# Kernel optimization log

Hardware: AMD Instinct MI355X
Metric: run time of the kernel (lower is better)

## Reference

```python
import jax, jax.numpy as jnp
import numpy as np

V, SMAX, D, L, H, F = 50257, 1024, 768, 12, 12, 3072
DH = D // H
SCALE = float(np.sqrt(DH))


def setup_inputs() -> dict:
    key = jax.random.key(0)
    ks = jax.random.split(key, 24)
    B, S = 2, 1024
    std = 0.02
    inp = {
        'input_ids': jax.random.randint(ks[0], (B, S), 0, V),
        'tok_emb': jax.random.normal(ks[1], (V, D), jnp.float32) * std,
        'pos_emb': jax.random.normal(ks[2], (SMAX, D), jnp.float32) * std,
        # stacked per-layer params (leading dim L)
        'Wq': jax.random.normal(ks[3], (L, D, D), jnp.float32) * std,
        'bq': jnp.zeros((L, D), jnp.float32),
        'Wk': jax.random.normal(ks[4], (L, D, D), jnp.float32) * std,
        'bk': jnp.zeros((L, D), jnp.float32),
        'Wv': jax.random.normal(ks[5], (L, D, D), jnp.float32) * std,
        'bv': jnp.zeros((L, D), jnp.float32),
        'Wo': jax.random.normal(ks[6], (L, D, D), jnp.float32) * std,
        'bo': jnp.zeros((L, D), jnp.float32),
        'ln1_g': jnp.ones((L, D), jnp.float32),
        'ln1_b': jnp.zeros((L, D), jnp.float32),
        'ln2_g': jnp.ones((L, D), jnp.float32),
        'ln2_b': jnp.zeros((L, D), jnp.float32),
        'W1': jax.random.normal(ks[7], (L, D, F), jnp.float32) * std,
        'b1': jnp.zeros((L, F), jnp.float32),
        'W2': jax.random.normal(ks[8], (L, F, D), jnp.float32) * std,
        'b2': jnp.zeros((L, D), jnp.float32),
        'lnf_g': jnp.ones((D,), jnp.float32),
        'lnf_b': jnp.zeros((D,), jnp.float32),
        'Whead': jax.random.normal(ks[9], (D, V), jnp.float32) * std,
    }
    return inp


def _layernorm(x, g, b, eps=1e-5):
    mu = jnp.mean(x, axis=-1, keepdims=True)
    var = jnp.var(x, axis=-1, keepdims=True)
    return (x - mu) * jax.lax.rsqrt(var + eps) * g + b


def _gpt_forward(input_ids, tok_emb, pos_emb, Wq, bq, Wk, bk, Wv, bv, Wo, bo,
                 ln1_g, ln1_b, ln2_g, ln2_b, W1, b1, W2, b2, lnf_g, lnf_b, Whead):
    B, S = input_ids.shape
    x = tok_emb[input_ids] + pos_emb[:S][None, :, :]  # (B,S,D)
    # additive causal mask: -inf above the diagonal
    idx = jnp.arange(S)
    neg_inf = jnp.finfo(x.dtype).min
    mask = jnp.where(idx[None, :] > idx[:, None], neg_inf, 0.0).astype(x.dtype)  # (S,S)

    def block(x, p):
        (wq, bq_, wk, bk_, wv, bv_, wo, bo_, g1, b1_, g2, b2_, w1, bb1, w2, bb2) = p
        h = _layernorm(x, g1, b1_)
        q = (h @ wq + bq_).reshape(B, S, H, DH)
        k = (h @ wk + bk_).reshape(B, S, H, DH)
        v = (h @ wv + bv_).reshape(B, S, H, DH)
        scores = jnp.einsum('bqhd,bkhd->bhqk', q, k) / SCALE + mask
        attn = jax.nn.softmax(scores, axis=-1)
        o = jnp.einsum('bhqk,bkhd->bqhd', attn, v).reshape(B, S, D)
        x = x + (o @ wo + bo_)
        h2 = _layernorm(x, g2, b2_)
        ffn = jax.nn.gelu(h2 @ w1 + bb1, approximate=False) @ w2 + bb2
        return x + ffn, None

    params = (Wq, bq, Wk, bk, Wv, bv, Wo, bo, ln1_g, ln1_b, ln2_g, ln2_b, W1, b1, W2, b2)
    x, _ = jax.lax.scan(block, x, params)
    x = _layernorm(x, lnf_g, lnf_b)
    return x @ Whead  # (B,S,V) logits


def reference(input_ids, tok_emb, pos_emb, Wq, bq, Wk, bk, Wv, bv, Wo, bo,
              ln1_g, ln1_b, ln2_g, ln2_b, W1, b1, W2, b2, lnf_g, lnf_b, Whead):
    return _gpt_forward(input_ids, tok_emb, pos_emb, Wq, bq, Wk, bk, Wv, bv, Wo, bo,
                        ln1_g, ln1_b, ln2_g, ln2_b, W1, b1, W2, b2, lnf_g, lnf_b, Whead)
```

## Files before the change

### kernel.cpp

```cpp
#include <hip/hip_runtime.h>
#include <hip/hip_bf16.h>
#include <cstdint>
#include <cstddef>

#define DEV __device__ __forceinline__

typedef __attribute__((ext_vector_type(8))) short short8;
typedef __attribute__((ext_vector_type(4))) short s16x4;
typedef __attribute__((ext_vector_type(4))) float f32x4;
typedef unsigned short u16;
typedef unsigned int u32;

static constexpr int Vv = 50257;
static constexpr int Dd = 768;
static constexpr int Ll = 12;
static constexpr int Hh = 12;
static constexpr int Ff = 3072;
static constexpr int Ss = 1024;
static constexpr int Bbatch = 2;
static constexpr int DHh = 64;
static constexpr int Mtok = Bbatch * Ss;
static constexpr int NQKV = 3 * Dd;
static constexpr int VPAD = 50304;

DEV u16 f2bf(float f){ u32 x; __builtin_memcpy(&x, &f, 4); x += 0x7fffu + ((x >> 16) & 1u); return (u16)(x >> 16); }

DEV void gld_lds16(const void* g, void* l){
  __builtin_amdgcn_global_load_lds((const __attribute__((address_space(1))) void*)g,
                                   (__attribute__((address_space(3))) void*)l, 16, 0, 0);
}

__global__ __launch_bounds__(256) void k_embed_ln(const int* __restrict__ ids, const float* __restrict__ tok,
                                                  const float* __restrict__ pos, const float* __restrict__ g,
                                                  const float* __restrict__ b, float* __restrict__ x,
                                                  u16* __restrict__ h){
  int t = blockIdx.x, tid = threadIdx.x;
  int id = ids[t];
  int s = t & (Ss - 1);
  const float* tr = tok + (size_t)id * Dd;
  const float* pr = pos + (size_t)s * Dd;
  float v0 = tr[tid] + pr[tid], v1 = tr[tid + 256] + pr[tid + 256], v2 = tr[tid + 512] + pr[tid + 512];
  float* xr = x + (size_t)t * Dd;
  xr[tid] = v0; xr[tid + 256] = v1; xr[tid + 512] = v2;
  float sm = v0 + v1 + v2, ss = v0 * v0 + v1 * v1 + v2 * v2;
  for (int o = 1; o < 64; o <<= 1){ sm += __shfl_xor(sm, o, 64); ss += __shfl_xor(ss, o, 64); }
  __shared__ float red[8];
  int w = tid >> 6, l = tid & 63;
  if (l == 0){ red[w] = sm; red[w + 4] = ss; }
  __syncthreads();
  sm = red[0] + red[1] + red[2] + red[3];
  ss = red[4] + red[5] + red[6] + red[7];
  float mu = sm * (1.0f / Dd);
  float var = ss * (1.0f / Dd) - mu * mu;
  float rs = rsqrtf(var + 1e-5f);
  u16* yr = h + (size_t)t * Dd;
  yr[tid]       = f2bf((v0 - mu) * rs * g[tid]       + b[tid]);
  yr[tid + 256] = f2bf((v1 - mu) * rs * g[tid + 256] + b[tid + 256]);
  yr[tid + 512] = f2bf((v2 - mu) * rs * g[tid + 512] + b[tid + 512]);
}

__global__ __launch_bounds__(256) void k_ln(const float* __restrict__ x, const float* __restrict__ g,
                                            const float* __restrict__ b, u16* __restrict__ y){
  int row = blockIdx.x, tid = threadIdx.x;
  const float* xr = x + (size_t)row * Dd;
  float v0 = xr[tid], v1 = xr[tid + 256], v2 = xr[tid + 512];
  float s = v0 + v1 + v2, ss = v0 * v0 + v1 * v1 + v2 * v2;
  for (int o = 1; o < 64; o <<= 1){ s += __shfl_xor(s, o, 64); ss += __shfl_xor(ss, o, 64); }
  __shared__ float red[8];
  int w = tid >> 6, l = tid & 63;
  if (l == 0){ red[w] = s; red[w + 4] = ss; }
  __syncthreads();
  s = red[0] + red[1] + red[2] + red[3];
  ss = red[4] + red[5] + red[6] + red[7];
  float mu = s * (1.0f / Dd);
  float var = ss * (1.0f / Dd) - mu * mu;
  float rs = rsqrtf(var + 1e-5f);
  u16* yr = y + (size_t)row * Dd;
  yr[tid]       = f2bf((v0 - mu) * rs * g[tid]       + b[tid]);
  yr[tid + 256] = f2bf((v1 - mu) * rs * g[tid + 256] + b[tid + 256]);
  yr[tid + 512] = f2bf((v2 - mu) * rs * g[tid + 512] + b[tid + 512]);
}

__global__ __launch_bounds__(256) void k_combineln(const float* __restrict__ p, const float* __restrict__ bias,
                                                   float* __restrict__ x, const float* __restrict__ g,
                                                   const float* __restrict__ b, u16* __restrict__ h){
  constexpr size_t SL = (size_t)Mtok * Dd;
  int row = blockIdx.x, tid = threadIdx.x;
  float* xr = x + (size_t)row * Dd;
  const float* p0 = p + (size_t)row * Dd;
  const float* p1 = p0 + SL;
  float v0 = xr[tid]       + p0[tid]       + p1[tid]       + bias[tid];
  float v1 = xr[tid + 256] + p0[tid + 256] + p1[tid + 256] + bias[tid + 256];
  float v2 = xr[tid + 512] + p0[tid + 512] + p1[tid + 512] + bias[tid + 512];
  xr[tid] = v0; xr[tid + 256] = v1; xr[tid + 512] = v2;
  float s = v0 + v1 + v2, ss = v0 * v0 + v1 * v1 + v2 * v2;
  for (int o = 1; o < 64; o <<= 1){ s += __shfl_xor(s, o, 64); ss += __shfl_xor(ss, o, 64); }
  __shared__ float red[8];
  int w = tid >> 6, l = tid & 63;
  if (l == 0){ red[w] = s; red[w + 4] = ss; }
  __syncthreads();
  s = red[0] + red[1] + red[2] + red[3];
  ss = red[4] + red[5] + red[6] + red[7];
  float mu = s * (1.0f / Dd);
  float var = ss * (1.0f / Dd) - mu * mu;
  float rs = rsqrtf(var + 1e-5f);
  u16* yr = h + (size_t)row * Dd;
  yr[tid]       = f2bf((v0 - mu) * rs * g[tid]       + b[tid]);
  yr[tid + 256] = f2bf((v1 - mu) * rs * g[tid + 256] + b[tid + 256]);
  yr[tid + 512] = f2bf((v2 - mu) * rs * g[tid + 512] + b[tid + 512]);
}

__global__ __launch_bounds__(256) void k_transpose(const float* __restrict__ src, u16* __restrict__ dst,
                                                   int R, int C, long smat, long dmat){
  __shared__ float tile[64][33];
  src += (size_t)blockIdx.z * smat;
  dst += (size_t)blockIdx.z * dmat;
  int c0 = blockIdx.x * 32, r0 = blockIdx.y * 64;
  int tid = threadIdx.x;
  int tc = tid & 31, tr = tid >> 5;
  #pragma unroll
  for (int i = 0; i < 8; i++){
    int r = tr + i * 8, c = c0 + tc;
    tile[r][tc] = (c < C) ? src[(size_t)(r0 + r) * C + c] : 0.0f;
  }
  __syncthreads();
  #pragma unroll
  for (int it = 0; it < 2; it++){
    int id = it * 256 + tid;
    int c = id & 31, rg = id >> 5, r = rg * 4;
    int cc = c0 + c;
    if (cc < C){
      s16x4 v = { (short)f2bf(tile[r][c]), (short)f2bf(tile[r + 1][c]),
                  (short)f2bf(tile[r + 2][c]), (short)f2bf(tile[r + 3][c]) };
      *(s16x4*)(dst + (size_t)cc * R + r0 + r) = v;
    }
  }
}

__global__ void k_biaspack(const float* __restrict__ bq, const float* __restrict__ bk,
                           const float* __restrict__ bv, float* __restrict__ o){
  int i = blockIdx.x * 256 + threadIdx.x;
  int col = i % NQKV, lay = i / NQKV;
  float v = (col < Dd) ? bq[lay * Dd + col]
          : (col < 2 * Dd) ? bk[lay * Dd + col - Dd]
          : bv[lay * Dd + col - 2 * Dd];
  o[i] = v;
}

template<int BM, int BN, int EPI>
__global__ __launch_bounds__(256) void k_gemmF(const u16* __restrict__ A, const u16* __restrict__ Bt,
    const float* __restrict__ bias, float* __restrict__ Cf, u16* __restrict__ Cb,
    u16* __restrict__ vt, int Nn, int MT, int NT){
  constexpr bool SPLIT = (EPI == 4);
  constexpr int KST  = SPLIT ? Ff : Dd;
  constexpr int KLEN = SPLIT ? (Ff / 2) : Dd;
  constexpr int nk = KLEN / 32;
  constexpr int HM = BM / 2, HN = BN / 2, FM = HM / 16, FN = HN / 16;
  constexpr int nA = (BM * 4) / 256, nB = (BN * 4) / 256;
  constexpr int ABYTE = BM * 64, BBYTE = BN * 64;
  __shared__ __align__(16) u16 ldsA[2 * BM * 32];
  __shared__ __align__(16) u16 ldsB[2 * BN * 32];
  int tid = threadIdx.x, wid = tid >> 6, l = tid & 63;
  int wm = wid >> 1, wn = wid & 1;
  int lr = l & 15, lc = l >> 4;
  int nwg = gridDim.x, dIdx = blockIdx.x;
  int L = (dIdx & 7) * (nwg >> 3) + (dIdx >> 3);
  int kidx = 0;
  if (SPLIT){ int per = MT * NT; kidx = L / per; L -= kidx * per; }
  int mtile = L % MT, ntile = L / MT;
  int m0 = mtile * BM, n0 = ntile * BN;
  int kbase = kidx * KLEN;

  const u16* gA[nA]; u16* dA[nA];
  const u16* gB[nB]; u16* dB[nB];
  #pragma unroll
  for (int i = 0; i < nA; i++){
    int id = i * 256 + tid, row = id >> 2, c = id & 3;
    int cs = c ^ ((row >> 1) & 3);
    gA[i] = A + (size_t)(m0 + row) * KST + kbase + cs * 8;
    dA[i] = ldsA + id * 8;
  }
  #pragma unroll
  for (int i = 0; i < nB; i++){
    int id = i * 256 + tid, row = id >> 2, c = id & 3;
    int cs = c ^ ((row >> 1) & 3);
    gB[i] = Bt + (size_t)(n0 + row) * KST + kbase + cs * 8;
    dB[i] = ldsB + id * 8;
  }
  int offA[FM], offB[FN];
  #pragma unroll
  for (int i = 0; i < FM; i++){
    int row = wm * HM + i * 16 + lr;
    offA[i] = row * 64 + ((lc ^ ((row >> 1) & 3)) << 4);
  }
  #pragma unroll
  for (int j = 0; j < FN; j++){
    int row = wn * HN + j * 16 + lr;
    offB[j] = row * 64 + ((lc ^ ((row >> 1) & 3)) << 4);
  }

  f32x4 acc[FM][FN];
  #pragma unroll
  for (int i = 0; i < FM; i++)
    #pragma unroll
    for (int j = 0; j < FN; j++) acc[i][j] = (f32x4)0.0f;

  auto stage = [&](int buf){
    #pragma unroll
    for (int i = 0; i < nA; i++){ gld_lds16(gA[i], (char*)dA[i] + buf * ABYTE); gA[i] += 32; }
    #pragma unroll
    for (int i = 0; i < nB; i++){ gld_lds16(gB[i], (char*)dB[i] + buf * BBYTE); gB[i] += 32; }
  };
  auto compute = [&](int buf){
    const char* bA = (const char*)ldsA + buf * ABYTE;
    const char* bB = (const char*)ldsB + buf * BBYTE;
    short8 af[FM], bfr[FN];
    #pragma unroll
    for (int i = 0; i < FM; i++) af[i] = *(const short8*)(bA + offA[i]);
    #pragma unroll
    for (int j = 0; j < FN; j++) bfr[j] = *(const short8*)(bB + offB[j]);
    #pragma unroll
    for (int i = 0; i < FM; i++)
      #pragma unroll
      for (int j = 0; j < FN; j++){
        if (EPI == 0)
          acc[i][j] = __builtin_amdgcn_mfma_f32_16x16x32_bf16(af[i], bfr[j], acc[i][j], 0, 0, 0);
        else
          acc[i][j] = __builtin_amdgcn_mfma_f32_16x16x32_bf16(bfr[j], af[i], acc[i][j], 0, 0, 0);
      }
  };

  stage(0);
  __syncthreads();
  #pragma unroll 1
  for (int t = 0; t < nk - 1; ++t){
    stage((t + 1) & 1);
    compute(t & 1);
    __syncthreads();
  }
  compute((nk - 1) & 1);

  if (EPI == 0){
    #pragma unroll
    for (int i = 0; i < FM; i++){
      #pragma unroll
      for (int j = 0; j < FN; j++){
        int col = n0 + wn * HN + j * 16 + lr;
        if (col >= Nn) continue;
        #pragma unroll
        for (int r = 0; r < 4; r++){
          int row = m0 + wm * HM + i * 16 + lc * 4 + r;
          Cf[(size_t)row * Nn + col] = acc[i][j][r];
        }
      }
    }
    return;
  }
  #pragma unroll
  for (int i = 0; i < FM; i++){
    int row = m0 + wm * HM + i * 16 + lr;
    #pragma unroll
    for (int j = 0; j < FN; j++){
      int c0 = n0 + wn * HN + j * 16 + lc * 4;
      f32x4 v = acc[i][j];
      if (EPI == 4){
        *(f32x4*)(Cf + (size_t)kidx * Mtok * Dd + (size_t)row * Dd + c0) = v;
        continue;
      }
      f32x4 bv = *(const f32x4*)(bias + c0);
      v = v + bv;
      if (EPI == 3){
        f32x4* p = (f32x4*)(Cf + (size_t)row * Nn + c0);
        *p = *p + v;
        continue;
      }
      if (EPI == 1 && c0 < Dd) v = v * 0.125f;
      if (EPI == 2){
        #pragma unroll
        for (int r = 0; r < 4; r++) v[r] = 0.5f * v[r] * (1.0f + erff(v[r] * 0.70710678118f));
      }
      u16 q0 = f2bf(v[0]), q1 = f2bf(v[1]), q2 = f2bf(v[2]), q3 = f2bf(v[3]);
      if (EPI == 1 && c0 >= 2 * Dd){
        int c2 = c0 - 2 * Dd, hh = c2 >> 6, dd2 = c2 & 63;
        int bb = row >> 10, ss2 = row & 1023;
        size_t base = ((size_t)((bb * Hh + hh) * DHh + dd2)) << 10;
        vt[base + ss2] = q0;
        vt[base + (1 << 10) + ss2] = q1;
        vt[base + (2 << 10) + ss2] = q2;
        vt[base + (3 << 10) + ss2] = q3;
      } else {
        s16x4 pv = { (short)q0, (short)q1, (short)q2, (short)q3 };
        *(s16x4*)(Cb + (size_t)row * Nn + c0) = pv;
      }
    }
  }
}

__global__ __launch_bounds__(256) void k_attn(const u16* __restrict__ qkv, const u16* __restrict__ vt,
                                              u16* __restrict__ o){
  __shared__ __align__(16) u16 ldsK[64 * 64];
  __shared__ __align__(16) u16 ldsV[64 * 64];
  __shared__ __align__(16) u16 ldsP[4][16 * 72];
  int bid = blockIdx.x;
  int iq = (Ss / 64) - 1 - (bid / (Bbatch * Hh));
  int bh = bid % (Bbatch * Hh);
  int b = bh / Hh, h = bh % Hh;
  int tid = threadIdx.x, wid = tid >> 6, l = tid & 63, lr = l & 15, lc = l >> 4;
  int nt = iq + 1;
  int qrow = b * Ss + iq * 64 + wid * 16 + lr;
  const u16* qp = qkv + (size_t)qrow * NQKV + h * DHh;
  short8 qf0 = *(const short8*)(qp + lc * 8);
  short8 qf1 = *(const short8*)(qp + 32 + lc * 8);

  const u16* gK[2]; const u16* gV[2]; u16* dK[2]; u16* dV[2];
  #pragma unroll
  for (int c = 0; c < 2; c++){
    int id = c * 256 + tid, row = id >> 3, ch = id & 7;
    int cs = ch ^ (row & 7);
    gK[c] = qkv + (size_t)(b * Ss + row) * NQKV + Dd + h * DHh + cs * 8;
    gV[c] = vt + ((size_t)(bh * DHh) + row) * Ss + cs * 8;
    dK[c] = ldsK + id * 8;
    dV[c] = ldsV + id * 8;
  }
  int koff[4][2];
  #pragma unroll
  for (int fn = 0; fn < 4; fn++){
    int kv = fn * 16 + lr;
    #pragma unroll
    for (int ks = 0; ks < 2; ks++){
      int ch = ks * 4 + lc;
      koff[fn][ks] = kv * 128 + ((ch ^ (kv & 7)) << 4);
    }
  }

  float mreg = -1e30f, lsum = 0.0f;
  f32x4 oacc[4];
  #pragma unroll
  for (int i = 0; i < 4; i++) oacc[i] = (f32x4)0.0f;
  u16* pbase = ldsP[wid];

  #pragma unroll 1
  for (int t = 0; t < nt; ++t){
    #pragma unroll
    for (int c = 0; c < 2; c++){ gld_lds16(gK[c], dK[c]); gK[c] += (size_t)64 * NQKV; }
    #pragma unroll
    for (int c = 0; c < 2; c++){ gld_lds16(gV[c], dV[c]); gV[c] += 64; }
    __syncthreads();
    f32x4 sc[4];
    __builtin_amdgcn_s_setprio(1);
    #pragma unroll
    for (int fn = 0; fn < 4; fn++){
      short8 kf0 = *(const short8*)((const char*)ldsK + koff[fn][0]);
      short8 kf1 = *(const short8*)((const char*)ldsK + koff[fn][1]);
      sc[fn] = __builtin_amdgcn_mfma_f32_16x16x32_bf16(kf0, qf0, (f32x4)0.0f, 0, 0, 0);
      sc[fn] = __builtin_amdgcn_mfma_f32_16x16x32_bf16(kf1, qf1, sc[fn], 0, 0, 0);
    }
    __builtin_amdgcn_s_setprio(0);
    if (t == iq){
      #pragma unroll
      for (int fn = 0; fn < 4; fn++)
        #pragma unroll
        for (int r = 0; r < 4; r++)
          if (fn * 16 + lc * 4 + r > wid * 16 + lr) sc[fn][r] = -1e30f;
    }
    float pm = sc[0][0];
    #pragma unroll
    for (int fn = 0; fn < 4; fn++)
      #pragma unroll
      for (int r = 0; r < 4; r++) pm = fmaxf(pm, sc[fn][r]);
    pm = fmaxf(pm, __shfl_xor(pm, 16, 64));
    pm = fmaxf(pm, __shfl_xor(pm, 32, 64));
    float mnew = fmaxf(mreg, pm);
    float alpha = __expf(mreg - mnew);
    mreg = mnew;
    float rs = 0.0f;
    #pragma unroll
    for (int fn = 0; fn < 4; fn++)
      #pragma unroll
      for (int r = 0; r < 4; r++){
        float p = __expf(sc[fn][r] - mnew);
        sc[fn][r] = p;
        rs += p;
      }
    rs += __shfl_xor(rs, 16, 64);
    rs += __shfl_xor(rs, 32, 64);
    lsum = lsum * alpha + rs;
    #pragma unroll
    for (int fn = 0; fn < 4; fn++){
      s16x4 pv = { (short)f2bf(sc[fn][0]), (short)f2bf(sc[fn][1]),
                   (short)f2bf(sc[fn][2]), (short)f2bf(sc[fn][3]) };
      *(s16x4*)((char*)pbase + lr * 144 + fn * 32 + lc * 8) = pv;
    }
    asm volatile("s_waitcnt lgkmcnt(0)" ::: "memory");
    __builtin_amdgcn_sched_barrier(0);
    #pragma unroll
    for (int fd = 0; fd < 4; fd++)
      #pragma unroll
      for (int r = 0; r < 4; r++) oacc[fd][r] *= alpha;
    short8 pa0 = *(const short8*)((const char*)pbase + lr * 144 + lc * 16);
    short8 pa1 = *(const short8*)((const char*)pbase + lr * 144 + 64 + lc * 16);
    __builtin_amdgcn_s_setprio(1);
    #pragma unroll
    for (int fd = 0; fd < 4; fd++){
      short8 vf0 = *(const short8*)((const char*)ldsV + koff[fd][0]);
      short8 vf1 = *(const short8*)((const char*)ldsV + koff[fd][1]);
      oacc[fd] = __builtin_amdgcn_mfma_f32_16x16x32_bf16(vf0, pa0, oacc[fd], 0, 0, 0);
      oacc[fd] = __builtin_amdgcn_mfma_f32_16x16x32_bf16(vf1, pa1, oacc[fd], 0, 0, 0);
    }
    __builtin_amdgcn_s_setprio(0);
    __syncthreads();
  }
  float inv = 1.0f / lsum;
  int rowg = b * Ss + iq * 64 + wid * 16 + lr;
  #pragma unroll
  for (int fd = 0; fd < 4; fd++){
    s16x4 ov = { (short)f2bf(oacc[fd][0] * inv), (short)f2bf(oacc[fd][1] * inv),
                 (short)f2bf(oacc[fd][2] * inv), (short)f2bf(oacc[fd][3] * inv) };
    *(s16x4*)(o + (size_t)rowg * Dd + h * DHh + fd * 16 + lc * 4) = ov;
  }
}

extern "C" void kernel_launch(void* const* d_in, const int* in_sizes, int n_in,
                              void* d_out, int out_size, void* d_ws, size_t ws_size,
                              hipStream_t stream){
  const int*   ids  = (const int*)d_in[0];
  const float* tok  = (const float*)d_in[1];
  const float* pos  = (const float*)d_in[2];
  const float* Wq   = (const float*)d_in[3];
  const float* bq   = (const float*)d_in[4];
  const float* Wk   = (const float*)d_in[5];
  const float* bk   = (const float*)d_in[6];
  const float* Wv   = (const float*)d_in[7];
  const float* bv   = (const float*)d_in[8];
  const float* Wo   = (const float*)d_in[9];
  const float* bo   = (const float*)d_in[10];
  const float* ln1g = (const float*)d_in[11];
  const float* ln1b = (const float*)d_in[12];
  const float* ln2g = (const float*)d_in[13];
  const float* ln2b = (const float*)d_in[14];
  const float* W1   = (const float*)d_in[15];
  const float* b1   = (const float*)d_in[16];
  const float* W2   = (const float*)d_in[17];
  const float* b2   = (const float*)d_in[18];
  const float* lnfg = (const float*)d_in[19];
  const float* lnfb = (const float*)d_in[20];
  const float* Wh   = (const float*)d_in[21];
  float* out = (float*)d_out;

  auto al = [](size_t x){ return (x + 255) & ~(size_t)255; };
  size_t off = 0;
  auto take = [&](size_t bytes){ size_t r = off; off = al(off + bytes); return r; };
  size_t o_x    = take((size_t)Mtok * Dd * 4);
  size_t o_h    = take((size_t)Mtok * Dd * 2);
  size_t o_qkv  = take((size_t)Mtok * NQKV * 2);
  size_t o_vt   = take((size_t)Bbatch * Hh * DHh * Ss * 2);
  size_t o_o    = take((size_t)Mtok * Dd * 2);
  size_t o_mid  = take((size_t)Mtok * Ff * 2);
  size_t o_bq   = take((size_t)Ll * NQKV * 4);
  size_t o_part = take((size_t)2 * Mtok * Dd * 4);
  size_t o_rot = off;
  size_t o_wqkv, o_wo, o_w1, o_w2, o_wh;
  bool full;
  {
    size_t t = off;
    o_wqkv = t; t = al(t + (size_t)Ll * NQKV * Dd * 2);
    o_wo   = t; t = al(t + (size_t)Ll * Dd * Dd * 2);
    o_w1   = t; t = al(t + (size_t)Ll * Ff * Dd * 2);
    o_w2   = t; t = al(t + (size_t)Ll * Dd * Ff * 2);
    o_wh   = t; t = al(t + (size_t)VPAD * Dd * 2);
    full = (t <= ws_size);
  }
  char* ws = (char*)d_ws;
  float* x    = (float*)(ws + o_x);
  u16*   h    = (u16*)(ws + o_h);
  u16*   qkvb = (u16*)(ws + o_qkv);
  u16*   vtb  = (u16*)(ws + o_vt);
  u16*   ob   = (u16*)(ws + o_o);
  u16*   midb = (u16*)(ws + o_mid);
  float* bqkvp= (float*)(ws + o_bq);
  float* part = (float*)(ws + o_part);
  u16* wqkvT = full ? (u16*)(ws + o_wqkv) : (u16*)(ws + o_rot);
  u16* woT   = full ? (u16*)(ws + o_wo)   : (u16*)(ws + o_rot);
  u16* w1T   = full ? (u16*)(ws + o_w1)   : (u16*)(ws + o_rot);
  u16* w2T   = full ? (u16*)(ws + o_w2)   : (u16*)(ws + o_rot);
  u16* whT   = full ? (u16*)(ws + o_wh)   : (u16*)(ws + o_rot);

  auto tpose = [&](const float* src, u16* dst, int R, int C, int nmat, long smat, long dmat){
    k_transpose<<<dim3((C + 31) / 32, R / 64, nmat), 256, 0, stream>>>(src, dst, R, C, smat, dmat);
  };

  k_biaspack<<<(Ll * NQKV) / 256, 256, 0, stream>>>(bq, bk, bv, bqkvp);
  k_embed_ln<<<Mtok, 256, 0, stream>>>(ids, tok, pos, ln1g, ln1b, x, h);

  if (full){
    tpose(Wq, wqkvT,              Dd, Dd, Ll, (long)Dd * Dd, (long)NQKV * Dd);
    tpose(Wk, wqkvT + Dd * Dd,    Dd, Dd, Ll, (long)Dd * Dd, (long)NQKV * Dd);
    tpose(Wv, wqkvT + 2 * Dd * Dd,Dd, Dd, Ll, (long)Dd * Dd, (long)NQKV * Dd);
    tpose(Wo, woT, Dd, Dd, Ll, (long)Dd * Dd, (long)Dd * Dd);
    tpose(W1, w1T, Dd, Ff, Ll, (long)Dd * Ff, (long)Ff * Dd);
    tpose(W2, w2T, Ff, Dd, Ll, (long)Ff * Dd, (long)Dd * Ff);
    tpose(Wh, whT, Dd, Vv, 1, 0, 0);
  }

  auto gemm_qkv = [&](const u16* Aop, const u16* Bop, const float* bias, u16* Cb){
    constexpr int MT = Mtok / 64, NT = NQKV / 128;
    k_gemmF<64, 128, 1><<<MT * NT, 256, 0, stream>>>(Aop, Bop, bias, nullptr, Cb, vtb, NQKV, MT, NT);
  };
  auto gemm_wo = [&](const u16* Aop, const u16* Bop, const float* bias, float* C){
    constexpr int MT = Mtok / 64, NT = Dd / 64;
    k_gemmF<64, 64, 3><<<MT * NT, 256, 0, stream>>>(Aop, Bop, bias, C, nullptr, nullptr, Dd, MT, NT);
  };
  auto gemm_ffn1 = [&](const u16* Aop, const u16* Bop, const float* bias, u16* Cb){
    constexpr int MT = Mtok / 64, NT = Ff / 128;
    k_gemmF<64, 128, 2><<<MT * NT, 256, 0, stream>>>(Aop, Bop, bias, nullptr, Cb, nullptr, Ff, MT, NT);
  };
  auto gemm_ffn2 = [&](const u16* Aop, const u16* Bop){
    constexpr int MT = Mtok / 64, NT = Dd / 64;
    k_gemmF<64, 64, 4><<<MT * NT * 2, 256, 0, stream>>>(Aop, Bop, nullptr, part, nullptr, nullptr, Dd, MT, NT);
  };
  auto gemm_head = [&](const u16* Aop, const u16* Bop, float* C){
    constexpr int MT = Mtok / 128, NT = VPAD / 128;
    k_gemmF<128, 128, 0><<<MT * NT, 256, 0, stream>>>(Aop, Bop, nullptr, C, nullptr, nullptr, Vv, MT, NT);
  };

  for (int l = 0; l < Ll; ++l){
    const u16* wqkvL = full ? wqkvT + (size_t)l * NQKV * Dd : wqkvT;
    const u16* woL   = full ? woT   + (size_t)l * Dd * Dd   : woT;
    const u16* w1L   = full ? w1T   + (size_t)l * Ff * Dd   : w1T;
    const u16* w2L   = full ? w2T   + (size_t)l * Dd * Ff   : w2T;
    if (!full){
      tpose(Wq + (size_t)l * Dd * Dd, wqkvT,              Dd, Dd, 1, 0, 0);
      tpose(Wk + (size_t)l * Dd * Dd, wqkvT + Dd * Dd,    Dd, Dd, 1, 0, 0);
      tpose(Wv + (size_t)l * Dd * Dd, wqkvT + 2 * Dd * Dd,Dd, Dd, 1, 0, 0);
    }
    gemm_qkv(h, wqkvL, bqkvp + l * NQKV, qkvb);
    k_attn<<<(Ss / 64) * Bbatch * Hh, 256, 0, stream>>>(qkvb, vtb, ob);
    if (!full) tpose(Wo + (size_t)l * Dd * Dd, woT, Dd, Dd, 1, 0, 0);
    gemm_wo(ob, woL, bo + l * Dd, x);
    k_ln<<<Mtok, 256, 0, stream>>>(x, ln2g + l * Dd, ln2b + l * Dd, h);
    if (!full) tpose(W1 + (size_t)l * Dd * Ff, w1T, Dd, Ff, 1, 0, 0);
    gemm_ffn1(h, w1L, b1 + l * Ff, midb);
    if (!full) tpose(W2 + (size_t)l * Ff * Dd, w2T, Ff, Dd, 1, 0, 0);
    gemm_ffn2(midb, w2L);
    const float* gN = (l + 1 < Ll) ? (ln1g + (l + 1) * Dd) : lnfg;
    const float* bN = (l + 1 < Ll) ? (ln1b + (l + 1) * Dd) : lnfb;
    k_combineln<<<Mtok, 256, 0, stream>>>(part, b2 + l * Dd, x, gN, bN, h);
  }
  if (!full) tpose(Wh, whT, Dd, Vv, 1, 0, 0);
  gemm_head(h, whT, out);
}
```

Measured before the change: 2.133 ms.

## Add dedicated 256x128 LM-head GEMM, widen attention KV tiles, use exp2 softmax

Adds a separate LM-head GEMM kernel with 512 threads, 256x128 tiles and an XCD-aware tile remap, replacing the generic 128x128 path and dropping the EPI==0 branch from the generic GEMM. Attention now processes 128 keys per iteration, halving loop trips and barriers, at the cost of more LDS and registers plus extra masked work on the diagonal tile. Softmax switches to exp2f, with the log2(e) factor folded into the Q scale (0.125 becomes 0.18033688).

```diff
diff --git a/kernel.cpp b/kernel.cpp
--- a/kernel.cpp
+++ b/kernel.cpp
@@ -222,12 +222,8 @@
     #pragma unroll
     for (int i = 0; i < FM; i++)
       #pragma unroll
-      for (int j = 0; j < FN; j++){
-        if (EPI == 0)
-          acc[i][j] = __builtin_amdgcn_mfma_f32_16x16x32_bf16(af[i], bfr[j], acc[i][j], 0, 0, 0);
-        else
-          acc[i][j] = __builtin_amdgcn_mfma_f32_16x16x32_bf16(bfr[j], af[i], acc[i][j], 0, 0, 0);
-      }
+      for (int j = 0; j < FN; j++)
+        acc[i][j] = __builtin_amdgcn_mfma_f32_16x16x32_bf16(bfr[j], af[i], acc[i][j], 0, 0, 0);
   };
 
   stage(0);
@@ -240,22 +236,6 @@
   }
   compute((nk - 1) & 1);
 
-  if (EPI == 0){
-    #pragma unroll
-    for (int i = 0; i < FM; i++){
-      #pragma unroll
-      for (int j = 0; j < FN; j++){
-        int col = n0 + wn * HN + j * 16 + lr;
-        if (col >= Nn) continue;
-        #pragma unroll
-        for (int r = 0; r < 4; r++){
-          int row = m0 + wm * HM + i * 16 + lc * 4 + r;
-          Cf[(size_t)row * Nn + col] = acc[i][j][r];
-        }
-      }
-    }
-    return;
-  }
   #pragma unroll
   for (int i = 0; i < FM; i++){
     int row = m0 + wm * HM + i * 16 + lr;
@@ -274,7 +254,7 @@
         *p = *p + v;
         continue;
       }
-      if (EPI == 1 && c0 < Dd) v = v * 0.125f;
+      if (EPI == 1 && c0 < Dd) v = v * 0.18033688f;
       if (EPI == 2){
         #pragma unroll
         for (int r = 0; r < 4; r++) v[r] = 0.5f * v[r] * (1.0f + erff(v[r] * 0.70710678118f));
@@ -296,35 +276,132 @@
   }
 }
 
+__global__ __launch_bounds__(512) void k_head(const u16* __restrict__ A, const u16* __restrict__ Bt,
+                                              float* __restrict__ Cf, int Nn, int MT, int NT){
+  constexpr int BM = 256, BN = 128, nk = Dd / 32;
+  constexpr int FM = 4, FN = 4;
+  constexpr int nA = 2, nB = 1;
+  constexpr int ABYTE = BM * 64, BBYTE = BN * 64;
+  __shared__ __align__(16) u16 ldsA[2 * BM * 32];
+  __shared__ __align__(16) u16 ldsB[2 * BN * 32];
+  int tid = threadIdx.x, wid = tid >> 6, l = tid & 63;
+  int wm = wid >> 1, wn = wid & 1;
+  int lr = l & 15, lc = l >> 4;
+  int nwg = gridDim.x, dIdx = blockIdx.x;
+  int L = (dIdx & 7) * (nwg >> 3) + (dIdx >> 3);
+  int mtile = L % MT, ntile = L / MT;
+  int m0 = mtile * BM, n0 = ntile * BN;
+
+  const u16* gA[nA]; u16* dA[nA];
+  const u16* gB[nB]; u16* dB[nB];
+  #pragma unroll
+  for (int i = 0; i < nA; i++){
+    int id = i * 512 + tid, row = id >> 2, c = id & 3;
+    int cs = c ^ ((row >> 1) & 3);
+    gA[i] = A + (size_t)(m0 + row) * Dd + cs * 8;
+    dA[i] = ldsA + id * 8;
+  }
+  {
+    int id = tid, row = id >> 2, c = id & 3;
+    int cs = c ^ ((row >> 1) & 3);
+    gB[0] = Bt + (size_t)(n0 + row) * Dd + cs * 8;
+    dB[0] = ldsB + id * 8;
+  }
+  int offA[FM], offB[FN];
+  #pragma unroll
+  for (int i = 0; i < FM; i++){
+    int row = wm * 64 + i * 16 + lr;
+    offA[i] = row * 64 + ((lc ^ ((row >> 1) & 3)) << 4);
+  }
+  #pragma unroll
+  for (int j = 0; j < FN; j++){
+    int row = wn * 64 + j * 16 + lr;
+    offB[j] = row * 64 + ((lc ^ ((row >> 1) & 3)) << 4);
+  }
+
+  f32x4 acc[FM][FN];
+  #pragma unroll
+  for (int i = 0; i < FM; i++)
+    #pragma unroll
+    for (int j = 0; j < FN; j++) acc[i][j] = (f32x4)0.0f;
+
+  auto stage = [&](int buf){
+    #pragma unroll
+    for (int i = 0; i < nA; i++){ gld_lds16(gA[i], (char*)dA[i] + buf * ABYTE); gA[i] += 32; }
+    gld_lds16(gB[0], (char*)dB[0] + buf * BBYTE); gB[0] += 32;
+  };
+  auto compute = [&](int buf){
+    const char* bA = (const char*)ldsA + buf * ABYTE;
+    const char* bB = (const char*)ldsB + buf * BBYTE;
+    short8 af[FM], bfr[FN];
+    #pragma unroll
+    for (int i = 0; i < FM; i++) af[i] = *(const short8*)(bA + offA[i]);
+    #pragma unroll
+    for (int j = 0; j < FN; j++) bfr[j] = *(const short8*)(bB + offB[j]);
+    #pragma unroll
+    for (int i = 0; i < FM; i++)
+      #pragma unroll
+      for (int j = 0; j < FN; j++)
+        acc[i][j] = __builtin_amdgcn_mfma_f32_16x16x32_bf16(af[i], bfr[j], acc[i][j], 0, 0, 0);
+  };
+
+  stage(0);
+  __syncthreads();
+  #pragma unroll 1
+  for (int t = 0; t < nk - 1; ++t){
+    stage((t + 1) & 1);
+    compute(t & 1);
+    __syncthreads();
+  }
+  compute((nk - 1) & 1);
+
+  #pragma unroll
+  for (int i = 0; i < FM; i++){
+    #pragma unroll
+    for (int j = 0; j < FN; j++){
+      int col = n0 + wn * 64 + j * 16 + lr;
+      if (col >= Nn) continue;
+      #pragma unroll
+      for (int r = 0; r < 4; r++){
+        int row = m0 + wm * 64 + i * 16 + lc * 4 + r;
+        Cf[(size_t)row * Nn + col] = acc[i][j][r];
+      }
+    }
+  }
+}
+
 __global__ __launch_bounds__(256) void k_attn(const u16* __restrict__ qkv, const u16* __restrict__ vt,
                                               u16* __restrict__ o){
-  __shared__ __align__(16) u16 ldsK[64 * 64];
-  __shared__ __align__(16) u16 ldsV[64 * 64];
-  __shared__ __align__(16) u16 ldsP[4][16 * 72];
+  constexpr int PSTR = 272;
+  __shared__ __align__(16) u16 ldsK[128 * 64];
+  __shared__ __align__(16) u16 ldsV[64 * 128];
+  __shared__ __align__(16) u16 ldsP[4][16 * 136];
   int bid = blockIdx.x;
   int iq = (Ss / 64) - 1 - (bid / (Bbatch * Hh));
   int bh = bid % (Bbatch * Hh);
   int b = bh / Hh, h = bh % Hh;
   int tid = threadIdx.x, wid = tid >> 6, l = tid & 63, lr = l & 15, lc = l >> 4;
-  int nt = iq + 1;
-  int qrow = b * Ss + iq * 64 + wid * 16 + lr;
-  const u16* qp = qkv + (size_t)qrow * NQKV + h * DHh;
+  int nt = (iq >> 1) + 1;
+  int qg = iq * 64 + wid * 16 + lr;
+  const u16* qp = qkv + (size_t)(b * Ss + qg) * NQKV + h * DHh;
   short8 qf0 = *(const short8*)(qp + lc * 8);
   short8 qf1 = *(const short8*)(qp + 32 + lc * 8);
 
-  const u16* gK[2]; const u16* gV[2]; u16* dK[2]; u16* dV[2];
-  #pragma unroll
-  for (int c = 0; c < 2; c++){
-    int id = c * 256 + tid, row = id >> 3, ch = id & 7;
-    int cs = ch ^ (row & 7);
-    gK[c] = qkv + (size_t)(b * Ss + row) * NQKV + Dd + h * DHh + cs * 8;
-    gV[c] = vt + ((size_t)(bh * DHh) + row) * Ss + cs * 8;
-    dK[c] = ldsK + id * 8;
-    dV[c] = ldsV + id * 8;
-  }
-  int koff[4][2];
-  #pragma unroll
-  for (int fn = 0; fn < 4; fn++){
+  const u16* gK[4]; const u16* gV[4]; u16* dK[4]; u16* dV[4];
+  #pragma unroll
+  for (int c = 0; c < 4; c++){
+    int idK = c * 256 + tid, rowK = idK >> 3, chK = idK & 7;
+    int csK = chK ^ (rowK & 7);
+    gK[c] = qkv + (size_t)(b * Ss + rowK) * NQKV + Dd + h * DHh + csK * 8;
+    dK[c] = ldsK + idK * 8;
+    int idV = c * 256 + tid, rowV = idV >> 4, chV = idV & 15;
+    int csV = chV ^ (rowV & 7);
+    gV[c] = vt + ((size_t)(bh * DHh) + rowV) * Ss + csV * 8;
+    dV[c] = ldsV + idV * 8;
+  }
+  int koff[8][2], voff[4][4];
+  #pragma unroll
+  for (int fn = 0; fn < 8; fn++){
     int kv = fn * 16 + lr;
     #pragma unroll
     for (int ks = 0; ks < 2; ks++){
@@ -332,6 +409,15 @@
       koff[fn][ks] = kv * 128 + ((ch ^ (kv & 7)) << 4);
     }
   }
+  #pragma unroll
+  for (int fd = 0; fd < 4; fd++){
+    int dd = fd * 16 + lr;
+    #pragma unroll
+    for (int ks = 0; ks < 4; ks++){
+      int ch = ks * 4 + lc;
+      voff[fd][ks] = dd * 256 + ((ch ^ (dd & 7)) << 4);
+    }
+  }
 
   float mreg = -1e30f, lsum = 0.0f;
   f32x4 oacc[4];
@@ -342,43 +428,43 @@
   #pragma unroll 1
   for (int t = 0; t < nt; ++t){
     #pragma unroll
-    for (int c = 0; c < 2; c++){ gld_lds16(gK[c], dK[c]); gK[c] += (size_t)64 * NQKV; }
-    #pragma unroll
-    for (int c = 0; c < 2; c++){ gld_lds16(gV[c], dV[c]); gV[c] += 64; }
+    for (int c = 0; c < 4; c++){ gld_lds16(gK[c], dK[c]); gK[c] += (size_t)128 * NQKV; }
+    #pragma unroll
+    for (int c = 0; c < 4; c++){ gld_lds16(gV[c], dV[c]); gV[c] += 128; }
     __syncthreads();
-    f32x4 sc[4];
+    f32x4 sc[8];
     __builtin_amdgcn_s_setprio(1);
     #pragma unroll
-    for (int fn = 0; fn < 4; fn++){
+    for (int fn = 0; fn < 8; fn++){
       short8 kf0 = *(const short8*)((const char*)ldsK + koff[fn][0]);
       short8 kf1 = *(const short8*)((const char*)ldsK + koff[fn][1]);
       sc[fn] = __builtin_amdgcn_mfma_f32_16x16x32_bf16(kf0, qf0, (f32x4)0.0f, 0, 0, 0);
       sc[fn] = __builtin_amdgcn_mfma_f32_16x16x32_bf16(kf1, qf1, sc[fn], 0, 0, 0);
     }
     __builtin_amdgcn_s_setprio(0);
-    if (t == iq){
-      #pragma unroll
-      for (int fn = 0; fn < 4; fn++)
+    if (t == nt - 1){
+      #pragma unroll
+      for (int fn = 0; fn < 8; fn++)
         #pragma unroll
         for (int r = 0; r < 4; r++)
-          if (fn * 16 + lc * 4 + r > wid * 16 + lr) sc[fn][r] = -1e30f;
+          if (t * 128 + fn * 16 + lc * 4 + r > qg) sc[fn][r] = -1e30f;
     }
     float pm = sc[0][0];
     #pragma unroll
-    for (int fn = 0; fn < 4; fn++)
+    for (int fn = 0; fn < 8; fn++)
       #pragma unroll
       for (int r = 0; r < 4; r++) pm = fmaxf(pm, sc[fn][r]);
     pm = fmaxf(pm, __shfl_xor(pm, 16, 64));
     pm = fmaxf(pm, __shfl_xor(pm, 32, 64));
     float mnew = fmaxf(mreg, pm);
-    float alpha = __expf(mreg - mnew);
+    float alpha = exp2f(mreg - mnew);
     mreg = mnew;
     float rs = 0.0f;
     #pragma unroll
-    for (int fn = 0; fn < 4; fn++)
+    for (int fn = 0; fn < 8; fn++)
       #pragma unroll
       for (int r = 0; r < 4; r++){
-        float p = __expf(sc[fn][r] - mnew);
+        float p = exp2f(sc[fn][r] - mnew);
         sc[fn][r] = p;
         rs += p;
       }
@@ -386,10 +472,10 @@
     rs += __shfl_xor(rs, 32, 64);
     lsum = lsum * alpha + rs;
     #pragma unroll
-    for (int fn = 0; fn < 4; fn++){
+    for (int fn = 0; fn < 8; fn++){
       s16x4 pv = { (short)f2bf(sc[fn][0]), (short)f2bf(sc[fn][1]),
                    (short)f2bf(sc[fn][2]), (short)f2bf(sc[fn][3]) };
-      *(s16x4*)((char*)pbase + lr * 144 + fn * 32 + lc * 8) = pv;
+      *(s16x4*)((char*)pbase + lr * PSTR + fn * 32 + lc * 8) = pv;
     }
     asm volatile("s_waitcnt lgkmcnt(0)" ::: "memory");
     __builtin_amdgcn_sched_barrier(0);
@@ -397,21 +483,23 @@
     for (int fd = 0; fd < 4; fd++)
       #pragma unroll
       for (int r = 0; r < 4; r++) oacc[fd][r] *= alpha;
-    short8 pa0 = *(const short8*)((const char*)pbase + lr * 144 + lc * 16);
-    short8 pa1 = *(const short8*)((const char*)pbase + lr * 144 + 64 + lc * 16);
+    short8 pa[4];
+    #pragma unroll
+    for (int ks = 0; ks < 4; ks++)
+      pa[ks] = *(const short8*)((const char*)pbase + lr * PSTR + ks * 64 + lc * 16);
     __builtin_amdgcn_s_setprio(1);
     #pragma unroll
-    for (int fd = 0; fd < 4; fd++){
-      short8 vf0 = *(const short8*)((const char*)ldsV + koff[fd][0]);
-      short8 vf1 = *(const short8*)((const char*)ldsV + koff[fd][1]);
-      oacc[fd] = __builtin_amdgcn_mfma_f32_16x16x32_bf16(vf0, pa0, oacc[fd], 0, 0, 0);
-      oacc[fd] = __builtin_amdgcn_mfma_f32_16x16x32_bf16(vf1, pa1, oacc[fd], 0, 0, 0);
-    }
+    for (int fd = 0; fd < 4; fd++)
+      #pragma unroll
+      for (int ks = 0; ks < 4; ks++){
+        short8 vf = *(const short8*)((const char*)ldsV + voff[fd][ks]);
+        oacc[fd] = __builtin_amdgcn_mfma_f32_16x16x32_bf16(vf, pa[ks], oacc[fd], 0, 0, 0);
+      }
     __builtin_amdgcn_s_setprio(0);
     __syncthreads();
   }
   float inv = 1.0f / lsum;
-  int rowg = b * Ss + iq * 64 + wid * 16 + lr;
+  int rowg = b * Ss + qg;
   #pragma unroll
   for (int fd = 0; fd < 4; fd++){
     s16x4 ov = { (short)f2bf(oacc[fd][0] * inv), (short)f2bf(oacc[fd][1] * inv),
@@ -519,8 +607,8 @@
     k_gemmF<64, 64, 4><<<MT * NT * 2, 256, 0, stream>>>(Aop, Bop, nullptr, part, nullptr, nullptr, Dd, MT, NT);
   };
   auto gemm_head = [&](const u16* Aop, const u16* Bop, float* C){
-    constexpr int MT = Mtok / 128, NT = VPAD / 128;
-    k_gemmF<128, 128, 0><<<MT * NT, 256, 0, stream>>>(Aop, Bop, nullptr, C, nullptr, nullptr, Vv, MT, NT);
+    constexpr int MT = Mtok / 256, NT = VPAD / 128;
+    k_head<<<MT * NT, 512, 0, stream>>>(Aop, Bop, C, Vv, MT, NT);
   };
 
   for (int l = 0; l < Ll; ++l){
```

Result: no change. 2.093 ms (median of 2 runs) (-1.9%).
